# Optimization experiments

Hardware: AMD Instinct MI355X
Metric: run time of the kernel (lower is better)

Reference implementation:

```python
import jax, jax.numpy as jnp
import numpy as np

B, S, F_IN, H = 128, 512, 64, 512
EPS = 1e-5  # torch BatchNorm1d default eps


def setup_inputs() -> dict:
    key = jax.random.key(0)
    ks = jax.random.split(key, 20)
    stdv = 1.0 / np.sqrt(H)
    u = lambda k, shape: jax.random.uniform(k, shape, jnp.float32, -stdv, stdv)
    return {
        "input_data": jax.random.normal(ks[0], (B, S, F_IN), jnp.float32),
        # MCLSTM params
        "W": u(ks[1], (F_IN, 4 * H + 5)),
        "U": u(ks[2], (H, 4 * H + 5)),
        "kernel1": u(ks[3], (1, 5 * H)),
        "bias": u(ks[4], (4 * H + 5,)),
        "bias1": u(ks[5], (2 * H,)),
        "rw1": u(ks[6], (H, H // 2)), "rb1": u(ks[7], (H // 2,)),
        "rw2": u(ks[8], (H // 2, H // 4)), "rb2": u(ks[9], (H // 4,)),
        "rbng": jnp.ones((H // 4,), jnp.float32), "rbnb": jnp.zeros((H // 4,), jnp.float32),
        "rw3": u(ks[10], (H // 4, 1)), "rb3": u(ks[11], (1,)),
        # domain classifier head (shared across c1..c5)
        "dw1": u(ks[12], (H, H // 2)), "db1": u(ks[13], (H // 2,)),
        "dbng": jnp.ones((H // 2,), jnp.float32), "dbnb": jnp.zeros((H // 2,), jnp.float32),
        "dw2": u(ks[14], (H // 2, 2)), "db2": u(ks[15], (2,)),
        "alpha": 1,
    }


def _batchnorm(x, g, b):
    # training-mode BatchNorm1d: biased batch stats
    m = jnp.mean(x, axis=0)
    v = jnp.var(x, axis=0)
    return (x - m) / jnp.sqrt(v + EPS) * g + b


def _mclstm_last(x, W, U, kernel1, bias, bias1):
    """Run the MCLSTM recurrence, returning last-step (h, c, c1..c5, d).
    Only the final timestep of each returned sequence is consumed by DANNModel,
    so we carry the per-step values instead of materializing [B,S,H] stacks."""
    bs = x.shape[0]
    s1, s2 = bias1[:H], bias1[H:2 * H]
    k = kernel1.reshape(5, H)  # kernel_1..kernel_5, each [H]

    def step(carry, x_t):
        h, c = carry[0], carry[1]
        gates = x_t @ W + h @ U + bias  # [B, 4H+5]
        i = jax.nn.sigmoid(gates[:, :H])
        f = jax.nn.sigmoid(gates[:, H:2 * H])
        g = jnp.tanh(gates[:, 2 * H:3 * H])
        o = jax.nn.sigmoid(gates[:, 3 * H:4 * H])
        d = jax.nn.softmax(jnp.tanh(gates[:, 4 * H:]), axis=1)  # [B,5]
        c1 = jnp.tanh(g)          # double tanh, faithful to source
        c5 = c
        c3 = f * c + i * g
        c2 = s2 * c3 + (1 - s2) * c1
        c4 = s1 * c3 + (1 - s1) * c5
        # torch.mm(d_j, kernel_j) is an outer product [B,1]x[1,H]
        c_new = ((d[:, 0:1] * k[0]) * c1 + (d[:, 1:2] * k[1]) * c2 +
                 (d[:, 2:3] * k[2]) * c3 + (d[:, 3:4] * k[3]) * c4 +
                 (d[:, 4:5] * k[4]) * c5)
        h_new = o * jnp.tanh(c_new)
        return (h_new, c_new, c1, c2, c3, c4, c5, d), None

    z = jnp.zeros((bs, H), x.dtype)
    init = (z, z, z, z, z, z, z, jnp.zeros((bs, 5), x.dtype))
    carry, _ = jax.lax.scan(step, init, jnp.swapaxes(x, 0, 1))
    return carry


def reference(input_data, W, U, kernel1, bias, bias1,
              rw1, rb1, rw2, rb2, rbng, rbnb, rw3, rb3,
              dw1, db1, dbng, dbnb, dw2, db2, alpha):
    h, c, c1, c2, c3, c4, c5, d = _mclstm_last(input_data, W, U, kernel1, bias, bias1)

    r = jax.nn.relu(h @ rw1 + rb1)
    r = jax.nn.relu(r @ rw2 + rb2)
    r = _batchnorm(r, rbng, rbnb)
    rul = r @ rw3 + rb3

    # domain classifier (ReverseLayerF is identity in forward)
    def dom(feat):
        y = jax.nn.relu(feat @ dw1 + db1)
        y = _batchnorm(y, dbng, dbnb)
        return jax.nn.log_softmax(y @ dw2 + db2, axis=1)

    return (rul, dom(c1), dom(c2), dom(c3), dom(c4), dom(c5), d)
```

## Files before the change

kernel.cpp:

```cpp
#include <hip/hip_runtime.h>
#include <hip/hip_bf16.h>
#include <math.h>

#define Bb   128
#define Ss   512
#define Ff   64
#define Hh   512
#define NGc  2053
#define Kk   576

#define OFF_HB    4096
#define OFF_HFIN  528384
#define OFF_CFIN  790528
#define OFF_R1    2101248
#define OFF_R2    2232320
#define OFF_Y1    2297856

typedef __attribute__((ext_vector_type(8))) short short8;
typedef __attribute__((ext_vector_type(4))) float f32x4;
typedef __attribute__((ext_vector_type(4))) int   i32x4a;

__device__ __forceinline__ unsigned short f2bf(float f) {
    union { float f; unsigned u; } v; v.f = f;
    unsigned r = v.u + 0x7fffu + ((v.u >> 16) & 1u);
    return (unsigned short)(r >> 16);
}

__device__ __forceinline__ float frcp(float x) { return __builtin_amdgcn_rcpf(x); }

__device__ __forceinline__ float ftanh(float x) {
    float ax = fabsf(x);
    float t  = __expf(-2.f * ax);
    float r  = (1.f - t) * frcp(1.f + t);
    return copysignf(r, x);
}
__device__ __forceinline__ float fsig(float x) {
    return frcp(1.f + __expf(-x));
}

#define HL8(T, a, a2)                                                  \
  asm volatile(                                                        \
    "global_load_dwordx4 %0, %8, off sc0 sc1\n\t"                      \
    "global_load_dwordx4 %1, %8, off offset:16 sc0 sc1\n\t"            \
    "global_load_dwordx4 %2, %8, off offset:2048 sc0 sc1\n\t"          \
    "global_load_dwordx4 %3, %8, off offset:2064 sc0 sc1\n\t"          \
    "global_load_dwordx4 %4, %9, off sc0 sc1\n\t"                      \
    "global_load_dwordx4 %5, %9, off offset:16 sc0 sc1\n\t"            \
    "global_load_dwordx4 %6, %9, off offset:2048 sc0 sc1\n\t"          \
    "global_load_dwordx4 %7, %9, off offset:2064 sc0 sc1\n\t"          \
    "s_waitcnt vmcnt(0)"                                               \
    : "=v"(T[0]), "=v"(T[1]), "=v"(T[2]), "=v"(T[3]),                  \
      "=v"(T[4]), "=v"(T[5]), "=v"(T[6]), "=v"(T[7])                   \
    : "v"(a), "v"(a2) : "memory")

__global__ __launch_bounds__(256, 1) void mclstm_main(
    const float* __restrict__ xin, const float* __restrict__ Wm,
    const float* __restrict__ Um,  const float* __restrict__ k1,
    const float* __restrict__ bias, const float* __restrict__ bias1,
    float* __restrict__ out, unsigned char* __restrict__ ws)
{
    __shared__ __align__(16) float predG[2][4][16][16][4];
    __shared__ __align__(16) float predD[2][5][16][4];

    const int tid   = threadIdx.x;
    const int bid   = blockIdx.x;
    const int g_id  = bid & 7;
    const int w_id  = bid >> 3;
    const int lane  = tid & 63;
    const int wv    = tid >> 6;
    const int j0    = w_id * 16;
    const int col16 = lane & 15;
    const int quad  = lane >> 4;

    float* hfin = (float*)(ws + OFF_HFIN);
    float* cfin = (float*)(ws + OFF_CFIN);

    short8 Bf[5][5];
#pragma unroll
    for (int i = 0; i < 4; ++i) {
        int kb = (wv * 4 + i) * 32 + quad * 8;
#pragma unroll
        for (int nt = 0; nt < 5; ++nt) {
            int col = (nt < 4) ? (nt * Hh + j0 + col16)
                               : ((col16 < 5) ? (4 * Hh + col16) : -1);
            short8 b;
#pragma unroll
            for (int j = 0; j < 8; ++j) {
                float v = (col >= 0) ? Um[(size_t)(kb + j) * NGc + col] : 0.f;
                b[j] = (short)f2bf(v);
            }
            Bf[1 + i][nt] = b;
        }
    }
    if (wv < 2) {
        int kb = wv * 32 + quad * 8;
#pragma unroll
        for (int nt = 0; nt < 5; ++nt) {
            int col = (nt < 4) ? (nt * Hh + j0 + col16)
                               : ((col16 < 5) ? (4 * Hh + col16) : -1);
            short8 b;
#pragma unroll
            for (int j = 0; j < 8; ++j) {
                float v = (col >= 0) ? Wm[(size_t)(kb + j) * NGc + col] : 0.f;
                b[j] = (short)f2bf(v);
            }
            Bf[0][nt] = b;
        }
    }

    const int rrow = tid >> 4, uu = tid & 15;
    const int u_g  = j0 + uu;
    const float bi = bias[0 * Hh + u_g], bf = bias[1 * Hh + u_g];
    const float bg = bias[2 * Hh + u_g], bo = bias[3 * Hh + u_g];
    float bd[5], kv[5];
#pragma unroll
    for (int c = 0; c < 5; ++c) { bd[c] = bias[4 * Hh + c]; kv[c] = k1[c * Hh + u_g]; }
    const float s1v = bias1[u_g], s2v = bias1[Hh + u_g];
    float cpreg = 0.f;

    const int kb_p = u_g >> 5, kin = u_g & 31;
    const unsigned pub_off = (unsigned)(kb_p * 2048 + (kin >> 3) * 512 + rrow * 32 + (kin & 7) * 4);

    __syncthreads();

    for (int t = 0; t < Ss; ++t) {
        char* hcur = (char*)ws + OFF_HB + (((t & 1) * 8 + g_id) * 32768);
        char* hnxt = (char*)ws + OFF_HB + ((((t + 1) & 1) * 8 + g_id) * 32768);
        const int pp = t & 1;

        f32x4 acc[5];
#pragma unroll
        for (int nt = 0; nt < 5; ++nt) { f32x4 z = {0.f, 0.f, 0.f, 0.f}; acc[nt] = z; }

        if (wv < 2) {
            short8 Ax;
            const float* p = xin + ((size_t)(16 * g_id + col16) * Ss + t) * Ff
                           + wv * 32 + quad * 8;
            f32x4 f0 = *(const f32x4*)(p);
            f32x4 f1 = *(const f32x4*)(p + 4);
#pragma unroll
            for (int j = 0; j < 4; ++j) {
                Ax[j]     = (short)f2bf(f0[j]);
                Ax[4 + j] = (short)f2bf(f1[j]);
            }
#pragma unroll
            for (int nt = 0; nt < 5; ++nt)
                acc[nt] = __builtin_amdgcn_mfma_f32_16x16x32_bf16(Ax, Bf[0][nt], acc[nt], 0, 0, 0);
        }

        i32x4a T[8];
        {
            unsigned long long hb = (unsigned long long)
                (hcur + (wv * 4) * 2048 + quad * 512 + col16 * 32);
            unsigned long long hb2 = hb + 4096;
            const unsigned expect = (unsigned)t << 16;
            for (int it = 0; it < (1 << 22); ++it) {
                HL8(T, hb, hb2);
                unsigned diff = 0u;
#pragma unroll
                for (int i = 0; i < 8; ++i)
#pragma unroll
                    for (int j = 0; j < 4; ++j)
                        diff |= ((unsigned)T[i][j]) ^ expect;
                if (__all((int)((diff >> 16) == 0u))) break;
            }
        }

#pragma unroll
        for (int i = 0; i < 4; ++i) {
            short8 a;
#pragma unroll
            for (int j = 0; j < 4; ++j) {
                a[j]     = (short)(T[2 * i][j] & 0xFFFF);
                a[4 + j] = (short)(T[2 * i + 1][j] & 0xFFFF);
            }
#pragma unroll
            for (int nt = 0; nt < 5; ++nt)
                acc[nt] = __builtin_amdgcn_mfma_f32_16x16x32_bf16(a, Bf[1 + i][nt], acc[nt], 0, 0, 0);
        }

#pragma unroll
        for (int j = 0; j < 4; ++j) {
            f32x4 g4 = {acc[0][j], acc[1][j], acc[2][j], acc[3][j]};
            *(f32x4*)&predG[pp][wv][quad * 4 + j][col16][0] = g4;
        }
        if (col16 < 5) {
#pragma unroll
            for (int j = 0; j < 4; ++j)
                predD[pp][col16][quad * 4 + j][wv] = acc[4][j];
        }
        __syncthreads();

        {
            f32x4 g4 = {bi, bf, bg, bo};
#pragma unroll
            for (int w = 0; w < 4; ++w) {
                f32x4 p = *(const f32x4*)&predG[pp][w][rrow][uu][0];
                g4 += p;
            }
            float dv[5];
#pragma unroll
            for (int c = 0; c < 5; ++c) {
                f32x4 dp = *(const f32x4*)&predD[pp][c][rrow][0];
                dv[c] = bd[c] + ((dp[0] + dp[1]) + (dp[2] + dp[3]));
            }
            float sden = 0.f;
#pragma unroll
            for (int c = 0; c < 5; ++c) { dv[c] = __expf(ftanh(dv[c])); sden += dv[c]; }
            float inv = frcp(sden);
#pragma unroll
            for (int c = 0; c < 5; ++c) dv[c] *= inv;

            float i_ = fsig(g4[0]);
            float f_ = fsig(g4[1]);
            float g_ = ftanh(g4[2]);
            float o_ = fsig(g4[3]);
            float c1v = ftanh(g_);
            float c5v = cpreg;
            float c3v = f_ * c5v + i_ * g_;
            float c2v = s2v * c3v + (1.f - s2v) * c1v;
            float c4v = s1v * c3v + (1.f - s1v) * c5v;
            float cn = dv[0] * kv[0] * c1v + dv[1] * kv[1] * c2v + dv[2] * kv[2] * c3v
                     + dv[3] * kv[3] * c4v + dv[4] * kv[4] * c5v;
            float hn = o_ * ftanh(cn);
            cpreg = cn;

            if (t < Ss - 1) {
                unsigned word = ((unsigned)(t + 1) << 16) | (unsigned)f2bf(hn);
                __hip_atomic_store((unsigned*)(hnxt + pub_off), word,
                                   __ATOMIC_RELAXED, __HIP_MEMORY_SCOPE_AGENT);
            } else {
                size_t off = (size_t)(16 * g_id + rrow) * Hh + u_g;
                hfin[off] = hn;
                cfin[0 * Bb * Hh + off] = c1v;
                cfin[1 * Bb * Hh + off] = c2v;
                cfin[2 * Bb * Hh + off] = c3v;
                cfin[3 * Bb * Hh + off] = c4v;
                cfin[4 * Bb * Hh + off] = c5v;
                if (w_id == 0 && uu == 0) {
#pragma unroll
                    for (int c = 0; c < 5; ++c)
                        out[1408 + (16 * g_id + rrow) * 5 + c] = dv[c];
                }
            }
        }
    }
}

__global__ __launch_bounds__(256) void stageA(const unsigned char* __restrict__ ws,
    const float* __restrict__ rw1, const float* __restrict__ rb1,
    const float* __restrict__ dw1, const float* __restrict__ db1)
{
    __shared__ float sW[512 * 17];
    const int tid = threadIdx.x;
    const int blk = blockIdx.x;
    const float* hfin = (const float*)(ws + OFF_HFIN);
    const float* cfin = (const float*)(ws + OFF_CFIN);
    float* r1 = (float*)(ws + OFF_R1);
    float* y1 = (float*)(ws + OFF_Y1);

    const float* src; const float* Wm; const float* bv; float* dst; int cblk;
    if (blk < 16) { src = hfin; Wm = rw1; bv = rb1; dst = r1; cblk = blk; }
    else {
        int hd = (blk - 16) >> 4; cblk = (blk - 16) & 15;
        src = cfin + (size_t)hd * Bb * Hh; Wm = dw1; bv = db1;
        dst = y1 + (size_t)hd * Bb * 256;
    }
    for (int e = tid; e < 512 * 16; e += 256) {
        int k = e >> 4, c = e & 15;
        sW[k * 17 + c] = Wm[(size_t)k * 256 + cblk * 16 + c];
    }
    __syncthreads();
    for (int e = tid; e < 128 * 16; e += 256) {
        int r = e >> 4, c = e & 15;
        float a = bv[cblk * 16 + c];
        const float* sp = src + (size_t)r * 512;
        for (int k = 0; k < 512; k += 4) {
            f32x4 h4 = *(const f32x4*)(sp + k);
            a += h4[0] * sW[(k + 0) * 17 + c] + h4[1] * sW[(k + 1) * 17 + c]
               + h4[2] * sW[(k + 2) * 17 + c] + h4[3] * sW[(k + 3) * 17 + c];
        }
        dst[(size_t)r * 256 + cblk * 16 + c] = fmaxf(a, 0.f);
    }
}

__global__ __launch_bounds__(256) void stageB(const unsigned char* __restrict__ ws,
    const float* __restrict__ rw2, const float* __restrict__ rb2)
{
    __shared__ float sW[256 * 17];
    const int tid = threadIdx.x;
    const int cblk = blockIdx.x;
    const float* r1 = (const float*)(ws + OFF_R1);
    float* r2 = (float*)(ws + OFF_R2);
    for (int e = tid; e < 256 * 16; e += 256) {
        int k = e >> 4, c = e & 15;
        sW[k * 17 + c] = rw2[(size_t)k * 128 + cblk * 16 + c];
    }
    __syncthreads();
    for (int e = tid; e < 128 * 16; e += 256) {
        int r = e >> 4, c = e & 15;
        float a = rb2[cblk * 16 + c];
        const float* sp = r1 + (size_t)r * 256;
        for (int k = 0; k < 256; k += 4) {
            f32x4 h4 = *(const f32x4*)(sp + k);
            a += h4[0] * sW[(k + 0) * 17 + c] + h4[1] * sW[(k + 1) * 17 + c]
               + h4[2] * sW[(k + 2) * 17 + c] + h4[3] * sW[(k + 3) * 17 + c];
        }
        r2[(size_t)r * 128 + cblk * 16 + c] = fmaxf(a, 0.f);
    }
}

__global__ __launch_bounds__(256) void stageC(const unsigned char* __restrict__ ws,
    const float* __restrict__ rbng, const float* __restrict__ rbnb,
    const float* __restrict__ rw3,  const float* __restrict__ rb3,
    const float* __restrict__ dbng, const float* __restrict__ dbnb,
    const float* __restrict__ dw2,  const float* __restrict__ db2,
    float* __restrict__ out)
{
    __shared__ float sc[256], sh[256];
    const int tid = threadIdx.x;
    const int blk = blockIdx.x;
    const float* r2 = (const float*)(ws + OFF_R2);
    const float* y1 = (const float*)(ws + OFF_Y1);
    if (blk == 0) {
        if (tid < 128) {
            int c = tid; float s = 0.f, s2 = 0.f;
            for (int r = 0; r < 128; ++r) { float x = r2[r * 128 + c]; s += x; s2 += x * x; }
            float m = s * (1.f / 128.f), v = s2 * (1.f / 128.f) - m * m;
            float sca = rbng[c] * rsqrtf(v + 1e-5f);
            sc[c] = sca; sh[c] = rbnb[c] - m * sca;
        }
        __syncthreads();
        if (tid < 128) {
            int r = tid; float a = rb3[0];
            for (int c = 0; c < 128; ++c)
                a += (r2[r * 128 + c] * sc[c] + sh[c]) * rw3[c];
            out[r] = a;
        }
    } else {
        int hd = blk - 1;
        const float* y = y1 + (size_t)hd * 128 * 256;
        {
            int c = tid; float s = 0.f, s2 = 0.f;
            for (int r = 0; r < 128; ++r) { float x = y[r * 256 + c]; s += x; s2 += x * x; }
            float m = s * (1.f / 128.f), v = s2 * (1.f / 128.f) - m * m;
            float sca = dbng[c] * rsqrtf(v + 1e-5f);
            sc[c] = sca; sh[c] = dbnb[c] - m * sca;
        }
        __syncthreads();
        if (tid < 128) {
            int r = tid;
            float z0 = db2[0], z1 = db2[1];
            for (int c = 0; c < 256; ++c) {
                float yn = y[r * 256 + c] * sc[c] + sh[c];
                z0 += yn * dw2[c * 2 + 0];
                z1 += yn * dw2[c * 2 + 1];
            }
            float mx = fmaxf(z0, z1);
            float ls = mx + logf(__expf(z0 - mx) + __expf(z1 - mx));
            out[128 + hd * 256 + r * 2 + 0] = z0 - ls;
            out[128 + hd * 256 + r * 2 + 1] = z1 - ls;
        }
    }
}

extern "C" void kernel_launch(void* const* d_in, const int* in_sizes, int n_in,
                              void* d_out, int out_size, void* d_ws, size_t ws_size,
                              hipStream_t stream) {
    const float* x    = (const float*)d_in[0];
    const float* Wm   = (const float*)d_in[1];
    const float* Um   = (const float*)d_in[2];
    const float* k1   = (const float*)d_in[3];
    const float* bias = (const float*)d_in[4];
    const float* b1   = (const float*)d_in[5];
    const float* rw1  = (const float*)d_in[6];
    const float* rb1  = (const float*)d_in[7];
    const float* rw2  = (const float*)d_in[8];
    const float* rb2  = (const float*)d_in[9];
    const float* rbng = (const float*)d_in[10];
    const float* rbnb = (const float*)d_in[11];
    const float* rw3  = (const float*)d_in[12];
    const float* rb3  = (const float*)d_in[13];
    const float* dw1  = (const float*)d_in[14];
    const float* db1  = (const float*)d_in[15];
    const float* dbng = (const float*)d_in[16];
    const float* dbnb = (const float*)d_in[17];
    const float* dw2  = (const float*)d_in[18];
    const float* db2  = (const float*)d_in[19];
    (void)in_sizes; (void)n_in; (void)out_size; (void)ws_size;

    hipMemsetAsync(d_ws, 0, OFF_HFIN, stream);

    mclstm_main<<<256, 256, 0, stream>>>(x, Wm, Um, k1, bias, b1,
                                         (float*)d_out, (unsigned char*)d_ws);
    stageA<<<96, 256, 0, stream>>>((const unsigned char*)d_ws, rw1, rb1, dw1, db1);
    stageB<<<8, 256, 0, stream>>>((const unsigned char*)d_ws, rw2, rb2);
    stageC<<<6, 256, 0, stream>>>((const unsigned char*)d_ws, rbng, rbnb, rw3, rb3,
                                  dbng, dbnb, dw2, db2, (float*)d_out);
}
```

Before: 1.404 ms.

## Add bounded fast-path polling on mirrored hidden-state buffer with sc0-only loads

```diff
diff --git a/kernel.cpp b/kernel.cpp
--- a/kernel.cpp
+++ b/kernel.cpp
@@ -15,6 +15,8 @@
 #define OFF_R1    2101248
 #define OFF_R2    2232320
 #define OFF_Y1    2297856
+#define OFF_MHB   2101248
+#define MHB_BYTES 524288
 
 typedef __attribute__((ext_vector_type(8))) short short8;
 typedef __attribute__((ext_vector_type(4))) float f32x4;
@@ -53,6 +55,21 @@
       "=v"(T[4]), "=v"(T[5]), "=v"(T[6]), "=v"(T[7])                   \
     : "v"(a), "v"(a2) : "memory")
 
+#define HL8S(T, a, a2)                                                 \
+  asm volatile(                                                        \
+    "global_load_dwordx4 %0, %8, off sc0\n\t"                          \
+    "global_load_dwordx4 %1, %8, off offset:16 sc0\n\t"                \
+    "global_load_dwordx4 %2, %8, off offset:2048 sc0\n\t"              \
+    "global_load_dwordx4 %3, %8, off offset:2064 sc0\n\t"              \
+    "global_load_dwordx4 %4, %9, off sc0\n\t"                          \
+    "global_load_dwordx4 %5, %9, off offset:16 sc0\n\t"                \
+    "global_load_dwordx4 %6, %9, off offset:2048 sc0\n\t"              \
+    "global_load_dwordx4 %7, %9, off offset:2064 sc0\n\t"              \
+    "s_waitcnt vmcnt(0)"                                               \
+    : "=v"(T[0]), "=v"(T[1]), "=v"(T[2]), "=v"(T[3]),                  \
+      "=v"(T[4]), "=v"(T[5]), "=v"(T[6]), "=v"(T[7])                   \
+    : "v"(a), "v"(a2) : "memory")
+
 __global__ __launch_bounds__(256, 1) void mclstm_main(
     const float* __restrict__ xin, const float* __restrict__ Wm,
     const float* __restrict__ Um,  const float* __restrict__ k1,
@@ -121,11 +138,15 @@
     const int kb_p = u_g >> 5, kin = u_g & 31;
     const unsigned pub_off = (unsigned)(kb_p * 2048 + (kin >> 3) * 512 + rrow * 32 + (kin & 7) * 4);
 
+    bool use_fast = true;
+
     __syncthreads();
 
     for (int t = 0; t < Ss; ++t) {
-        char* hcur = (char*)ws + OFF_HB + (((t & 1) * 8 + g_id) * 32768);
-        char* hnxt = (char*)ws + OFF_HB + ((((t + 1) & 1) * 8 + g_id) * 32768);
+        char* hcur = (char*)ws + OFF_HB  + (((t & 1) * 8 + g_id) * 32768);
+        char* hnxt = (char*)ws + OFF_HB  + ((((t + 1) & 1) * 8 + g_id) * 32768);
+        char* mcur = (char*)ws + OFF_MHB + (((t & 1) * 8 + g_id) * 32768);
+        char* mnxt = (char*)ws + OFF_MHB + ((((t + 1) & 1) * 8 + g_id) * 32768);
         const int pp = t & 1;
 
         f32x4 acc[5];
@@ -150,19 +171,39 @@
 
         i32x4a T[8];
         {
-            unsigned long long hb = (unsigned long long)
-                (hcur + (wv * 4) * 2048 + quad * 512 + col16 * 32);
-            unsigned long long hb2 = hb + 4096;
             const unsigned expect = (unsigned)t << 16;
-            for (int it = 0; it < (1 << 22); ++it) {
-                HL8(T, hb, hb2);
-                unsigned diff = 0u;
-#pragma unroll
-                for (int i = 0; i < 8; ++i)
-#pragma unroll
-                    for (int j = 0; j < 4; ++j)
-                        diff |= ((unsigned)T[i][j]) ^ expect;
-                if (__all((int)((diff >> 16) == 0u))) break;
+            bool got = false;
+            if (use_fast) {
+                unsigned long long mb = (unsigned long long)
+                    (mcur + (wv * 4) * 2048 + quad * 512 + col16 * 32);
+                unsigned long long mb2 = mb + 4096;
+                const int bound = (t == 1) ? 1024 : 256;
+                for (int it = 0; it < bound; ++it) {
+                    HL8S(T, mb, mb2);
+                    unsigned diff = 0u;
+#pragma unroll
+                    for (int i = 0; i < 8; ++i)
+#pragma unroll
+                        for (int j = 0; j < 4; ++j)
+                            diff |= ((unsigned)T[i][j]) ^ expect;
+                    if (__all((int)((diff >> 16) == 0u))) { got = true; break; }
+                }
+                if (!got) use_fast = false;
+            }
+            if (!got) {
+                unsigned long long hb = (unsigned long long)
+                    (hcur + (wv * 4) * 2048 + quad * 512 + col16 * 32);
+                unsigned long long hb2 = hb + 4096;
+                for (int it = 0; it < (1 << 22); ++it) {
+                    HL8(T, hb, hb2);
+                    unsigned diff = 0u;
+#pragma unroll
+                    for (int i = 0; i < 8; ++i)
+#pragma unroll
+                        for (int j = 0; j < 4; ++j)
+                            diff |= ((unsigned)T[i][j]) ^ expect;
+                    if (__all((int)((diff >> 16) == 0u))) break;
+                }
             }
         }
 
@@ -227,6 +268,7 @@
 
             if (t < Ss - 1) {
                 unsigned word = ((unsigned)(t + 1) << 16) | (unsigned)f2bf(hn);
+                *(volatile unsigned*)(mnxt + pub_off) = word;
                 __hip_atomic_store((unsigned*)(hnxt + pub_off), word,
                                    __ATOMIC_RELAXED, __HIP_MEMORY_SCOPE_AGENT);
             } else {
@@ -390,6 +432,7 @@
     (void)in_sizes; (void)n_in; (void)out_size; (void)ws_size;
 
     hipMemsetAsync(d_ws, 0, OFF_HFIN, stream);
+    hipMemsetAsync((char*)d_ws + OFF_MHB, 0, MHB_BYTES, stream);
 
     mclstm_main<<<256, 256, 0, stream>>>(x, Wm, Um, k1, bias, b1,
                                          (float*)d_out, (unsigned char*)d_ws);
```

Result: faster. 1.356 ms (-3.4%).

## Double-buffer h spin-poll loads and prefetch next-step input row

Applied to the files above, without the earlier changes.

```diff
diff --git a/kernel.cpp b/kernel.cpp
--- a/kernel.cpp
+++ b/kernel.cpp
@@ -38,7 +38,7 @@
     return frcp(1.f + __expf(-x));
 }
 
-#define HL8(T, a, a2)                                                  \
+#define HL8_ISS(T, a, a2)                                              \
   asm volatile(                                                        \
     "global_load_dwordx4 %0, %8, off sc0 sc1\n\t"                      \
     "global_load_dwordx4 %1, %8, off offset:16 sc0 sc1\n\t"            \
@@ -47,10 +47,26 @@
     "global_load_dwordx4 %4, %9, off sc0 sc1\n\t"                      \
     "global_load_dwordx4 %5, %9, off offset:16 sc0 sc1\n\t"            \
     "global_load_dwordx4 %6, %9, off offset:2048 sc0 sc1\n\t"          \
-    "global_load_dwordx4 %7, %9, off offset:2064 sc0 sc1\n\t"          \
-    "s_waitcnt vmcnt(0)"                                               \
+    "global_load_dwordx4 %7, %9, off offset:2064 sc0 sc1"              \
     : "=v"(T[0]), "=v"(T[1]), "=v"(T[2]), "=v"(T[3]),                  \
       "=v"(T[4]), "=v"(T[5]), "=v"(T[6]), "=v"(T[7])                   \
+    : "v"(a), "v"(a2) : "memory")
+
+#define HL8_ISSW(Tn, To, a, a2)                                        \
+  asm volatile(                                                        \
+    "global_load_dwordx4 %0, %16, off sc0 sc1\n\t"                     \
+    "global_load_dwordx4 %1, %16, off offset:16 sc0 sc1\n\t"           \
+    "global_load_dwordx4 %2, %16, off offset:2048 sc0 sc1\n\t"         \
+    "global_load_dwordx4 %3, %16, off offset:2064 sc0 sc1\n\t"         \
+    "global_load_dwordx4 %4, %17, off sc0 sc1\n\t"                     \
+    "global_load_dwordx4 %5, %17, off offset:16 sc0 sc1\n\t"           \
+    "global_load_dwordx4 %6, %17, off offset:2048 sc0 sc1\n\t"         \
+    "global_load_dwordx4 %7, %17, off offset:2064 sc0 sc1\n\t"         \
+    "s_waitcnt vmcnt(8)"                                               \
+    : "=v"(Tn[0]), "=v"(Tn[1]), "=v"(Tn[2]), "=v"(Tn[3]),              \
+      "=v"(Tn[4]), "=v"(Tn[5]), "=v"(Tn[6]), "=v"(Tn[7]),              \
+      "+v"(To[0]), "+v"(To[1]), "+v"(To[2]), "+v"(To[3]),              \
+      "+v"(To[4]), "+v"(To[5]), "+v"(To[6]), "+v"(To[7])               \
     : "v"(a), "v"(a2) : "memory")
 
 __global__ __launch_bounds__(256, 1) void mclstm_main(
@@ -121,6 +137,13 @@
     const int kb_p = u_g >> 5, kin = u_g & 31;
     const unsigned pub_off = (unsigned)(kb_p * 2048 + (kin >> 3) * 512 + rrow * 32 + (kin & 7) * 4);
 
+    const float* xbase = xin + (size_t)(16 * g_id + col16) * Ss * Ff + wv * 32 + quad * 8;
+    f32x4 xf0 = {0.f, 0.f, 0.f, 0.f}, xf1 = {0.f, 0.f, 0.f, 0.f};
+    if (wv < 2) {
+        xf0 = *(const f32x4*)(xbase);
+        xf1 = *(const f32x4*)(xbase + 4);
+    }
+
     __syncthreads();
 
     for (int t = 0; t < Ss; ++t) {
@@ -134,36 +157,53 @@
 
         if (wv < 2) {
             short8 Ax;
-            const float* p = xin + ((size_t)(16 * g_id + col16) * Ss + t) * Ff
-                           + wv * 32 + quad * 8;
-            f32x4 f0 = *(const f32x4*)(p);
-            f32x4 f1 = *(const f32x4*)(p + 4);
 #pragma unroll
             for (int j = 0; j < 4; ++j) {
-                Ax[j]     = (short)f2bf(f0[j]);
-                Ax[4 + j] = (short)f2bf(f1[j]);
+                Ax[j]     = (short)f2bf(xf0[j]);
+                Ax[4 + j] = (short)f2bf(xf1[j]);
             }
 #pragma unroll
             for (int nt = 0; nt < 5; ++nt)
                 acc[nt] = __builtin_amdgcn_mfma_f32_16x16x32_bf16(Ax, Bf[0][nt], acc[nt], 0, 0, 0);
         }
 
-        i32x4a T[8];
+        i32x4a TA[8], TB[8];
         {
             unsigned long long hb = (unsigned long long)
                 (hcur + (wv * 4) * 2048 + quad * 512 + col16 * 32);
             unsigned long long hb2 = hb + 4096;
             const unsigned expect = (unsigned)t << 16;
-            for (int it = 0; it < (1 << 22); ++it) {
-                HL8(T, hb, hb2);
+            bool useA = true;
+            HL8_ISS(TA, hb, hb2);
+            for (int it = 0; it < (1 << 21); ++it) {
+                HL8_ISSW(TB, TA, hb, hb2);
                 unsigned diff = 0u;
 #pragma unroll
                 for (int i = 0; i < 8; ++i)
 #pragma unroll
                     for (int j = 0; j < 4; ++j)
-                        diff |= ((unsigned)T[i][j]) ^ expect;
-                if (__all((int)((diff >> 16) == 0u))) break;
-            }
+                        diff |= ((unsigned)TA[i][j]) ^ expect;
+                if (__all((int)((diff >> 16) == 0u))) { useA = true; break; }
+                HL8_ISSW(TA, TB, hb, hb2);
+                diff = 0u;
+#pragma unroll
+                for (int i = 0; i < 8; ++i)
+#pragma unroll
+                    for (int j = 0; j < 4; ++j)
+                        diff |= ((unsigned)TB[i][j]) ^ expect;
+                if (__all((int)((diff >> 16) == 0u))) { useA = false; break; }
+            }
+            asm volatile("s_waitcnt vmcnt(0)" ::: "memory");
+            if (!useA) {
+#pragma unroll
+                for (int i = 0; i < 8; ++i) TA[i] = TB[i];
+            }
+        }
+
+        if (wv < 2 && t + 1 < Ss) {
+            const float* p = xbase + (size_t)(t + 1) * Ff;
+            xf0 = *(const f32x4*)(p);
+            xf1 = *(const f32x4*)(p + 4);
         }
 
 #pragma unroll
@@ -171,8 +211,8 @@
             short8 a;
 #pragma unroll
             for (int j = 0; j < 4; ++j) {
-                a[j]     = (short)(T[2 * i][j] & 0xFFFF);
-                a[4 + j] = (short)(T[2 * i + 1][j] & 0xFFFF);
+                a[j]     = (short)(TA[2 * i][j] & 0xFFFF);
+                a[4 + j] = (short)(TA[2 * i + 1][j] & 0xFFFF);
             }
 #pragma unroll
             for (int nt = 0; nt < 5; ++nt)
```

After: 1.530 ms. +8.9%, slower.
